# Kernel tuning notes

Hardware: AMD Instinct MI355X
Metric: run time of the kernel (lower is better)

Reference implementation:

```python
import jax, jax.numpy as jnp
import numpy as np

T, N, D = 8, 2048, 64
H, NH = 128, 4        # hidden_dim, num_heads (flax default num_heads=4)
HD = H // NH
TE = 16               # time_embedding_dim
OUT = 64              # final output_dim
E = D + TE            # enhanced node feature dim


def _params(key):
    ks = jax.random.split(key, 16)
    s = 0.05
    w = lambda k, shape: jax.random.normal(k, shape, jnp.float32) * s
    return dict(
        time_freq=w(ks[0], (T, TE // 2)) * 2.0,
        Wq=w(ks[1], (T, E, H)), bq=jnp.zeros((T, H), jnp.float32),
        Wk=w(ks[2], (T, E, H)), bk=jnp.zeros((T, H), jnp.float32),
        Wv=w(ks[3], (T, E, H)), bv=jnp.zeros((T, H), jnp.float32),
        ln_g=jnp.ones((T, H), jnp.float32), ln_b=jnp.zeros((T, H), jnp.float32),
        W1=w(ks[4], (T, H, 2 * H)), b1=jnp.zeros((T, 2 * H), jnp.float32),
        W2=w(ks[5], (T, 2 * H, H)), b2=jnp.zeros((T, H), jnp.float32),
        Wr=w(ks[6], (T, 2 * H, H)), br=jnp.zeros((T, H), jnp.float32),
        Wz=w(ks[7], (T, 2 * H, H)), bz=jnp.zeros((T, H), jnp.float32),
        Wn=w(ks[8], (T, 2 * H, H)), bn=jnp.zeros((T, H), jnp.float32),
        Wout=w(ks[9], (H, OUT)), bout=jnp.zeros((OUT,), jnp.float32),
    )


def setup_inputs() -> dict:
    key = jax.random.key(0)
    k0, k1, k2, k3, kp = jax.random.split(key, 5)
    inp = dict(
        node_sequence=jax.random.normal(k0, (T, N, D), jnp.float32),
        adjacency_sequence=(jax.random.uniform(k1, (T, N, N)) < 0.02).astype(jnp.float32),
        timestamps=jax.random.uniform(k2, (T, N), jnp.float32) * 100.0,
        edge_sequence=jax.random.randint(k3, (T, 32768, 2), 0, N),  # unused in math
    )
    inp.update(_params(kp))
    return inp


def _forward(node_sequence, adjacency_sequence, timestamps, time_freq,
             Wq, bq, Wk, bk, Wv, bv, ln_g, ln_b, W1, b1, W2, b2,
             Wr, br, Wz, bz, Wn, bn, Wout, bout):
    eye = jnp.eye(N, dtype=jnp.float32)
    inv_sqrt_hd = np.float32(1.0 / np.sqrt(HD))

    def step(h, xs):
        (nodes, adj, ts, tf, wq, bq_, wk, bk_, wv, bv_, g, b,
         w1, b1_, w2, b2_, wr, br_, wz, bz_, wn, bn_) = xs
        # sinusoidal time encoding -> enhanced node features [N, D+TE]
        ang = ts[:, None] * tf[None, :]
        enh = jnp.concatenate([nodes, jnp.sin(ang), jnp.cos(ang)], axis=-1)
        # the original builds per-head Dense projections in a Python loop;
        # concatenating them equals one [E,H] projection split into heads
        q = (enh @ wq + bq_).reshape(N, NH, HD)
        k = (enh @ wk + bk_).reshape(N, NH, HD)
        v = (enh @ wv + bv_).reshape(N, NH, HD)
        scores = jnp.einsum('nhd,mhd->hnm', q, k) * inv_sqrt_hd  # [NH,N,N]
        decay = jnp.exp(-jnp.abs(ts[:, None] - ts[None, :]) / 10.0)
        scores = scores * decay[None]
        mask = (adj + eye) > 0
        scores = jnp.where(mask[None], scores, -jnp.inf)
        attn = jax.nn.softmax(scores, axis=-1)
        mh = jnp.einsum('hnm,mhd->nhd', attn, v).reshape(N, H)
        # residual skipped: mh dim (128) != enhanced dim (80), as in source
        mu = mh.mean(-1, keepdims=True)
        var = mh.var(-1, keepdims=True)
        mh = (mh - mu) * jax.lax.rsqrt(var + 1e-6) * g + b  # LayerNorm eps=1e-6
        ff = jax.nn.gelu(mh @ w1 + b1_) @ w2 + b2_  # inner output_dim == hidden_dim
        # GRU cell
        hx = jnp.concatenate([h, ff], axis=-1)
        r = jax.nn.sigmoid(hx @ wr + br_)
        z = jax.nn.sigmoid(hx @ wz + bz_)
        n_ = jnp.tanh(jnp.concatenate([r * h, ff], axis=-1) @ wn + bn_)
        return (1.0 - z) * n_ + z * h, None

    xs = (node_sequence, adjacency_sequence, timestamps, time_freq,
          Wq, bq, Wk, bk, Wv, bv, ln_g, ln_b, W1, b1, W2, b2,
          Wr, br, Wz, bz, Wn, bn)
    h0 = jnp.zeros((N, H), jnp.float32)
    h, _ = jax.lax.scan(step, h0, xs)
    return h @ Wout + bout  # [N, OUT]


def reference(node_sequence, adjacency_sequence, timestamps, edge_sequence,
              time_freq, Wq, bq, Wk, bk, Wv, bv, ln_g, ln_b,
              W1, b1, W2, b2, Wr, br, Wz, bz, Wn, bn, Wout, bout):
    # edge_sequence is accepted by the original forward but never used
    return _forward(node_sequence, adjacency_sequence, timestamps, time_freq,
                    Wq, bq, Wk, bk, Wv, bv, ln_g, ln_b, W1, b1, W2, b2,
                    Wr, br, Wz, bz, Wn, bn, Wout, bout)
```

## Files before the change

### kernel.cpp

```cpp
#include <hip/hip_runtime.h>
#include <math.h>

#define T 8
#define N 2048
#define D 64
#define H 128
#define NH 4
#define HD 32
#define TE 16
#define OUT 64
#define E 80
#define NBCAP 128

typedef float f4v __attribute__((ext_vector_type(4)));
typedef __attribute__((ext_vector_type(8))) short bf16x8;
typedef __attribute__((ext_vector_type(4))) float f32x4;

__device__ __forceinline__ float gelu_tanh(float x){
    float x3 = x*x*x;
    float t = tanhf(0.7978845608028654f*(x + 0.044715f*x3));
    return 0.5f*x*(1.0f+t);
}
__device__ __forceinline__ float sigmoidf_(float x){ return 1.0f/(1.0f+expf(-x)); }
__device__ __forceinline__ unsigned short f2bf(float x){
    unsigned u = __float_as_uint(x);
    return (unsigned short)((u + 0x7FFFu + ((u>>16)&1u)) >> 16);
}
__device__ __forceinline__ float bf2f(unsigned short x){
    return __uint_as_float(((unsigned)x) << 16);
}

__global__ __launch_bounds__(256) void k_compact(
    const float* __restrict__ adj, unsigned short* __restrict__ nb, int* __restrict__ cnt)
{
    int wid  = threadIdx.x >> 6;
    int lane = threadIdx.x & 63;
    int row  = blockIdx.x*4 + wid;
    int n = row & 2047;
    const f4v* arow4 = (const f4v*)(adj + (size_t)row*(size_t)N);

    f4v a4[8];
    #pragma unroll
    for (int it=0; it<8; it++) a4[it] = __builtin_nontemporal_load(arow4 + it*64 + lane);

    unsigned short* nbr = nb + (size_t)row*NBCAP;
    int c = 0;
    unsigned long long lt = (1ull<<lane)-1ull;
    #pragma unroll
    for (int it = 0; it < 8; it++){
        int m0 = it*256 + lane*4;
        bool f0 = (a4[it].x>0.f) || (m0   == n);
        bool f1 = (a4[it].y>0.f) || (m0+1 == n);
        bool f2 = (a4[it].z>0.f) || (m0+2 == n);
        bool f3 = (a4[it].w>0.f) || (m0+3 == n);
        unsigned long long b0=__ballot(f0), b1=__ballot(f1), b2=__ballot(f2), b3=__ballot(f3);
        int before = __popcll(b0&lt)+__popcll(b1&lt)+__popcll(b2&lt)+__popcll(b3&lt);
        int pos = c + before;
        if (f0 && pos<NBCAP) nbr[pos] = (unsigned short)(m0  );  pos += f0;
        if (f1 && pos<NBCAP) nbr[pos] = (unsigned short)(m0+1);  pos += f1;
        if (f2 && pos<NBCAP) nbr[pos] = (unsigned short)(m0+2);  pos += f2;
        if (f3 && pos<NBCAP) nbr[pos] = (unsigned short)(m0+3);  pos += f3;
        c += __popcll(b0)+__popcll(b1)+__popcll(b2)+__popcll(b3);
    }
    if (lane == 0) cnt[row] = (c > NBCAP) ? NBCAP : c;
}

__global__ __launch_bounds__(64) void k_wswz(
    const float* __restrict__ W1, const float* __restrict__ W2,
    const float* __restrict__ Wr, const float* __restrict__ Wz, const float* __restrict__ Wn,
    unsigned short* __restrict__ W1s, unsigned short* __restrict__ W2s,
    unsigned short* __restrict__ Wrs, unsigned short* __restrict__ Wzs, unsigned short* __restrict__ Wns,
    unsigned short* __restrict__ Wrt, unsigned short* __restrict__ Wzt, unsigned short* __restrict__ Wnt)
{
    int b = blockIdx.x;
    const float* src; unsigned short* dst; int NT,KB,ncol,koff;
    if (b < 512)      {          src=W1; dst=W1s; NT=16; KB=4; ncol=256; koff=0;   }
    else if (b < 1024){ b-=512;  src=W2; dst=W2s; NT=8;  KB=8; ncol=128; koff=0;   }
    else if (b < 1280){ b-=1024; src=Wr; dst=Wrs; NT=8;  KB=4; ncol=128; koff=128; }
    else if (b < 1536){ b-=1280; src=Wz; dst=Wzs; NT=8;  KB=4; ncol=128; koff=128; }
    else if (b < 1792){ b-=1536; src=Wn; dst=Wns; NT=8;  KB=4; ncol=128; koff=128; }
    else if (b < 2048){ b-=1792; src=Wr; dst=Wrt; NT=8;  KB=4; ncol=128; koff=0;   }
    else if (b < 2304){ b-=2048; src=Wz; dst=Wzt; NT=8;  KB=4; ncol=128; koff=0;   }
    else              { b-=2304; src=Wn; dst=Wnt; NT=8;  KB=4; ncol=128; koff=0;   }
    int fpt = NT*KB;
    int t = b / fpt, rem = b % fpt, nt = rem / KB, kb = rem % KB;
    int lane = threadIdx.x;
    int kk = koff + kb*32 + (lane>>4)*8;
    int n  = nt*16 + (lane&15);
    const float* s = src + (size_t)t*32768;
    bf16x8 o;
    #pragma unroll
    for (int j=0;j<8;j++) o[j] = (short)f2bf(s[(size_t)(kk+j)*ncol + n]);
    *(bf16x8*)(dst + ((size_t)b*64 + lane)*8) = o;
}

__global__ __launch_bounds__(256) void k_qkv(
    const float* __restrict__ nodes, const float* __restrict__ ts, const float* __restrict__ tf,
    const float* __restrict__ Wq, const float* __restrict__ bq,
    const float* __restrict__ Wk, const float* __restrict__ bk,
    const float* __restrict__ Wv, const float* __restrict__ bv,
    float* __restrict__ q, float* __restrict__ k, float* __restrict__ v)
{
    const int BR = 16;
    __shared__ float A[BR*E];
    int t  = blockIdx.x >> 7;
    int n0 = (blockIdx.x & 127) * BR;
    int tid = threadIdx.x;
    for (int idx = tid; idx < BR*E; idx += 256){
        int r = idx / E, e = idx - r*E;
        int n = n0 + r;
        float val;
        if (e < D) val = nodes[((size_t)(t*N+n))*D + e];
        else {
            int j = (e - D) & 7;
            float ang = ts[t*N+n] * tf[t*(TE/2)+j];
            val = (e < D+8) ? sinf(ang) : cosf(ang);
        }
        A[idx] = val;
    }
    __syncthreads();
    for (int jj = tid; jj < 3*H; jj += 256){
        int sel = jj >> 7, j = jj & 127;
        const float* W = (sel==0?Wq:(sel==1?Wk:Wv)) + (size_t)t*E*H;
        const float* B = (sel==0?bq:(sel==1?bk:bv)) + t*H;
        float acc[BR];
        float bias = B[j];
        #pragma unroll
        for (int r=0;r<BR;r++) acc[r]=bias;
        for (int e=0;e<E;e+=4){
            float w0=W[(e+0)*H+j], w1=W[(e+1)*H+j], w2=W[(e+2)*H+j], w3=W[(e+3)*H+j];
            #pragma unroll
            for (int r=0;r<BR;r++){
                float4 a = *(const float4*)&A[r*E+e];
                acc[r] += a.x*w0 + a.y*w1 + a.z*w2 + a.w*w3;
            }
        }
        float* outp = (sel==0?q:(sel==1?k:v));
        #pragma unroll
        for (int r=0;r<BR;r++) outp[((size_t)(t*N+n0+r))*H + j] = acc[r];
    }
}

__global__ __launch_bounds__(256) void k_attn(
    const unsigned short* __restrict__ nb, const int* __restrict__ cntp,
    const float* __restrict__ ts,
    const float* __restrict__ q, const float* __restrict__ k, const float* __restrict__ v,
    const float* __restrict__ ln_g, const float* __restrict__ ln_b,
    float* __restrict__ mhn)
{
    __shared__ unsigned short nb_s[4][NBCAP];
    __shared__ float sc_s[4][64][NH];
    __shared__ float qrow_s[4][H];

    int wid  = threadIdx.x >> 6;
    int lane = threadIdx.x & 63;
    int t = blockIdx.x & 7;
    int n = (blockIdx.x >> 3)*4 + wid;
    int row = t*N + n;
    size_t rowbase = (size_t)row;
    float tsn = ts[row];
    int cnt = cntp[row];

    for (int i = lane; i < cnt; i += 64) nb_s[wid][i] = nb[rowbase*NBCAP + i];
    qrow_s[wid][lane]    = q[rowbase*H + lane];
    qrow_s[wid][lane+64] = q[rowbase*H + lane + 64];
    __builtin_amdgcn_wave_barrier();

    const float inv_sqrt_hd = 0.17677669529663687f;
    const float NEG = -3.402823466e38f;
    int g   = lane >> 4;
    int l16 = lane & 15;
    int hd  = l16 >> 2;
    int hh16 = lane >> 4;

    f4v q0 = *(const f4v*)&qrow_s[wid][l16*8];
    f4v q1 = *(const f4v*)&qrow_s[wid][l16*8+4];

    float mR0=NEG,mR1=NEG,mR2=NEG,mR3=NEG;
    float sR0=0.f,sR1=0.f,sR2=0.f,sR3=0.f;
    f4v accA = {0.f,0.f,0.f,0.f}, accB = {0.f,0.f,0.f,0.f};

    for (int cb = 0; cb < cnt; cb += 64){
        int cc = min(64, cnt - cb);
        for (int i0 = 0; i0 < cc; i0 += 4){
            int jn = i0 + g;
            bool act = jn < cc;
            float part = 0.f;
            int m = 0;
            if (act){
                m = nb_s[wid][cb + jn];
                const f4v* kp = (const f4v*)(k + ((size_t)t*N + m)*H + l16*8);
                f4v k0 = kp[0], k1 = kp[1];
                part = q0.x*k0.x + q0.y*k0.y + q0.z*k0.z + q0.w*k0.w
                     + q1.x*k1.x + q1.y*k1.y + q1.z*k1.z + q1.w*k1.w;
            }
            part += __shfl_xor(part, 1);
            part += __shfl_xor(part, 2);
            if (act && (l16 & 3) == 0){
                float dt = fabsf(tsn - ts[t*N + m]);
                float w  = expf(-dt*0.1f) * inv_sqrt_hd;
                sc_s[wid][jn][l16>>2] = part * w;
            }
        }
        __builtin_amdgcn_wave_barrier();
        float mx = NEG;
        for (int i = l16; i < cc; i += 16) mx = fmaxf(mx, sc_s[wid][i][hh16]);
        #pragma unroll
        for (int off=8; off; off>>=1) mx = fmaxf(mx, __shfl_xor(mx, off, 16));
        float h0m=__shfl(mx,0), h1m=__shfl(mx,16), h2m=__shfl(mx,32), h3m=__shfl(mx,48);
        float n0=fmaxf(mR0,h0m), n1=fmaxf(mR1,h1m), n2=fmaxf(mR2,h2m), n3=fmaxf(mR3,h3m);
        float e0=expf(mR0-n0), e1=expf(mR1-n1), e2=expf(mR2-n2), e3=expf(mR3-n3);
        float nh = (hh16==0)?n0:((hh16==1)?n1:((hh16==2)?n2:n3));
        float sum = 0.f;
        for (int i = l16; i < cc; i += 16){
            float p = expf(sc_s[wid][i][hh16] - nh);
            sc_s[wid][i][hh16] = p;
            sum += p;
        }
        #pragma unroll
        for (int off=8; off; off>>=1) sum += __shfl_xor(sum, off, 16);
        float su0=__shfl(sum,0), su1=__shfl(sum,16), su2=__shfl(sum,32), su3=__shfl(sum,48);
        sR0 = sR0*e0 + su0; sR1 = sR1*e1 + su1;
        sR2 = sR2*e2 + su2; sR3 = sR3*e3 + su3;
        mR0=n0; mR1=n1; mR2=n2; mR3=n3;
        float eh = (hd==0)?e0:((hd==1)?e1:((hd==2)?e2:e3));
        accA *= eh; accB *= eh;
        __builtin_amdgcn_wave_barrier();
        for (int i0 = 0; i0 < cc; i0 += 4){
            int jn = i0 + g;
            if (jn < cc){
                int m = nb_s[wid][cb + jn];
                const f4v* vp = (const f4v*)(v + ((size_t)t*N + m)*H + l16*8);
                f4v v0 = vp[0], v1 = vp[1];
                float p = sc_s[wid][jn][hd];
                accA += p * v0;
                accB += p * v1;
            }
        }
        __builtin_amdgcn_wave_barrier();
    }

    #pragma unroll
    for (int off = 16; off <= 32; off <<= 1){
        accA.x += __shfl_xor(accA.x, off); accA.y += __shfl_xor(accA.y, off);
        accA.z += __shfl_xor(accA.z, off); accA.w += __shfl_xor(accA.w, off);
        accB.x += __shfl_xor(accB.x, off); accB.y += __shfl_xor(accB.y, off);
        accB.z += __shfl_xor(accB.z, off); accB.w += __shfl_xor(accB.w, off);
    }
    float sh = (hd==0)?sR0:((hd==1)?sR1:((hd==2)?sR2:sR3));
    float inv = 1.f / sh;
    accA *= inv; accB *= inv;

    float ls = accA.x+accA.y+accA.z+accA.w + accB.x+accB.y+accB.z+accB.w;
    #pragma unroll
    for (int off=8; off; off>>=1) ls += __shfl_xor(ls, off, 16);
    float mu = ls * (1.f/128.f);
    f4v dA = accA - mu, dB = accB - mu;
    float vs = dA.x*dA.x+dA.y*dA.y+dA.z*dA.z+dA.w*dA.w
             + dB.x*dB.x+dB.y*dB.y+dB.z*dB.z+dB.w*dB.w;
    #pragma unroll
    for (int off=8; off; off>>=1) vs += __shfl_xor(vs, off, 16);
    float rs = rsqrtf(vs*(1.f/128.f) + 1e-6f);

    if (g == 0){
        const f4v* gp = (const f4v*)(ln_g + t*H + l16*8);
        const f4v* bp = (const f4v*)(ln_b + t*H + l16*8);
        f4v g0 = gp[0], g1 = gp[1], b0 = bp[0], b1 = bp[1];
        f4v o0 = dA*rs*g0 + b0;
        f4v o1 = dB*rs*g1 + b1;
        f4v* op = (f4v*)(mhn + rowbase*H + l16*8);
        op[0] = o0; op[1] = o1;
    }
}

#define ULD 264
__global__ __launch_bounds__(256) void k_ffpre(
    const float* __restrict__ mhn,
    const unsigned short* __restrict__ W1s, const float* __restrict__ b1,
    const unsigned short* __restrict__ W2s, const float* __restrict__ b2,
    const unsigned short* __restrict__ Wrs, const float* __restrict__ br,
    const unsigned short* __restrict__ Wzs, const float* __restrict__ bz,
    const unsigned short* __restrict__ Wns, const float* __restrict__ bn,
    unsigned short* __restrict__ fr, unsigned short* __restrict__ fz, unsigned short* __restrict__ fn)
{
    __shared__ unsigned short U_lds[32*ULD];
    int tid = threadIdx.x;
    int w = tid >> 6, lane = tid & 63;
    int t = blockIdx.x & 7;
    int n0 = (blockIdx.x >> 3) * 32;
    int li = lane & 15, ls = lane >> 4;

    bf16x8 af[2][4];
    const float* Abase = mhn + (size_t)(t*N + n0)*H;
    #pragma unroll
    for (int mt=0; mt<2; mt++){
        #pragma unroll
        for (int kb=0; kb<4; kb++){
            const float* p = Abase + (size_t)(mt*16 + li)*H + kb*32 + ls*8;
            float4 x0 = *(const float4*)p;
            float4 x1 = *(const float4*)(p+4);
            bf16x8 a;
            a[0]=(short)f2bf(x0.x); a[1]=(short)f2bf(x0.y); a[2]=(short)f2bf(x0.z); a[3]=(short)f2bf(x0.w);
            a[4]=(short)f2bf(x1.x); a[5]=(short)f2bf(x1.y); a[6]=(short)f2bf(x1.z); a[7]=(short)f2bf(x1.w);
            af[mt][kb] = a;
        }
    }

    const bf16x8* W1f = (const bf16x8*)W1s;
    #pragma unroll
    for (int u=0; u<4; u++){
        int nt = w*4 + u;
        f32x4 c0 = {0.f,0.f,0.f,0.f}, c1 = {0.f,0.f,0.f,0.f};
        #pragma unroll
        for (int kb=0; kb<4; kb++){
            bf16x8 b = W1f[((t*16 + nt)*4 + kb)*64 + lane];
            c0 = __builtin_amdgcn_mfma_f32_16x16x32_bf16(af[0][kb], b, c0, 0,0,0);
            c1 = __builtin_amdgcn_mfma_f32_16x16x32_bf16(af[1][kb], b, c1, 0,0,0);
        }
        float bias = b1[t*256 + nt*16 + li];
        #pragma unroll
        for (int i=0;i<4;i++){
            U_lds[(     ls*4+i)*ULD + nt*16 + li] = f2bf(gelu_tanh(c0[i] + bias));
            U_lds[(16 + ls*4+i)*ULD + nt*16 + li] = f2bf(gelu_tanh(c1[i] + bias));
        }
    }
    __syncthreads();

    const bf16x8* W2f = (const bf16x8*)W2s;
    f32x4 c2[2][2];
    #pragma unroll
    for (int u=0;u<2;u++){ c2[u][0] = (f32x4){0.f,0.f,0.f,0.f}; c2[u][1] = (f32x4){0.f,0.f,0.f,0.f}; }
    for (int kb=0; kb<8; kb++){
        bf16x8 a0 = *(const bf16x8*)&U_lds[(     li)*ULD + kb*32 + ls*8];
        bf16x8 a1 = *(const bf16x8*)&U_lds[(16 + li)*ULD + kb*32 + ls*8];
        #pragma unroll
        for (int u=0; u<2; u++){
            int nt = w*2 + u;
            bf16x8 b = W2f[((t*8 + nt)*8 + kb)*64 + lane];
            c2[u][0] = __builtin_amdgcn_mfma_f32_16x16x32_bf16(a0, b, c2[u][0], 0,0,0);
            c2[u][1] = __builtin_amdgcn_mfma_f32_16x16x32_bf16(a1, b, c2[u][1], 0,0,0);
        }
    }
    __syncthreads();
    #pragma unroll
    for (int u=0; u<2; u++){
        int nt = w*2 + u;
        float bias = b2[t*128 + nt*16 + li];
        #pragma unroll
        for (int i=0;i<4;i++){
            U_lds[(     ls*4+i)*ULD + nt*16 + li] = f2bf(c2[u][0][i] + bias);
            U_lds[(16 + ls*4+i)*ULD + nt*16 + li] = f2bf(c2[u][1][i] + bias);
        }
    }
    __syncthreads();

    bf16x8 aF[2][4];
    #pragma unroll
    for (int mt=0; mt<2; mt++)
        #pragma unroll
        for (int kb=0; kb<4; kb++)
            aF[mt][kb] = *(const bf16x8*)&U_lds[(mt*16 + li)*ULD + kb*32 + ls*8];

    #pragma unroll
    for (int u=0; u<6; u++){
        int unit = w*6 + u;
        int gate = unit >> 3, nt = unit & 7;
        const bf16x8* Wf = (const bf16x8*)(gate==0 ? Wrs : (gate==1 ? Wzs : Wns));
        const float*  Bv = gate==0 ? br : (gate==1 ? bz : bn);
        unsigned short* outp = gate==0 ? fr : (gate==1 ? fz : fn);
        f32x4 c0 = {0.f,0.f,0.f,0.f}, c1 = {0.f,0.f,0.f,0.f};
        #pragma unroll
        for (int kb=0; kb<4; kb++){
            bf16x8 b = Wf[((t*8 + nt)*4 + kb)*64 + lane];
            c0 = __builtin_amdgcn_mfma_f32_16x16x32_bf16(aF[0][kb], b, c0, 0,0,0);
            c1 = __builtin_amdgcn_mfma_f32_16x16x32_bf16(aF[1][kb], b, c1, 0,0,0);
        }
        float bias = Bv[t*128 + nt*16 + li];
        #pragma unroll
        for (int i=0;i<4;i++){
            outp[(size_t)(t*N + n0 +      ls*4+i)*H + nt*16 + li] = f2bf(c0[i] + bias);
            outp[(size_t)(t*N + n0 + 16 + ls*4+i)*H + nt*16 + li] = f2bf(c1[i] + bias);
        }
    }
}

#define HLD 132
__global__ __launch_bounds__(256) void k_gru_mfma(
    const unsigned short* __restrict__ fr, const unsigned short* __restrict__ fz,
    const unsigned short* __restrict__ fn,
    const unsigned short* __restrict__ Wrt, const unsigned short* __restrict__ Wzt,
    const unsigned short* __restrict__ Wnt,
    const float* __restrict__ Wout, const float* __restrict__ bout,
    float* __restrict__ out)
{
    __shared__ unsigned short fLDS[3*8*16*H];
    __shared__ float Hs[16*HLD], Zl[16*HLD], RH[16*HLD];
    int tid = threadIdx.x;
    int w = tid >> 6, lane = tid & 63;
    int li = lane & 15, ls = lane >> 4;
    int n0 = blockIdx.x * 16;
    int gateA = w >> 1;

    {
        const unsigned short* g0 = fr; const unsigned short* g1 = fz; const unsigned short* g2 = fn;
        #pragma unroll
        for (int t=0; t<T; t++){
            *(bf16x8*)&fLDS[(0*8+t)*2048 + tid*8] = *(const bf16x8*)(g0 + ((size_t)t*N+n0)*H + tid*8);
            *(bf16x8*)&fLDS[(1*8+t)*2048 + tid*8] = *(const bf16x8*)(g1 + ((size_t)t*N+n0)*H + tid*8);
            *(bf16x8*)&fLDS[(2*8+t)*2048 + tid*8] = *(const bf16x8*)(g2 + ((size_t)t*N+n0)*H + tid*8);
        }
    }
    for (int idx = tid; idx < 16*HLD; idx += 256) Hs[idx] = 0.f;
    __syncthreads();

    for (int t = 0; t < T; t++){
        bf16x8 af[4];
        #pragma unroll
        for (int kb=0; kb<4; kb++){
            const float* p = &Hs[li*HLD + kb*32 + ls*8];
            float4 x0 = *(const float4*)p, x1 = *(const float4*)(p+4);
            bf16x8 a;
            a[0]=(short)f2bf(x0.x); a[1]=(short)f2bf(x0.y); a[2]=(short)f2bf(x0.z); a[3]=(short)f2bf(x0.w);
            a[4]=(short)f2bf(x1.x); a[5]=(short)f2bf(x1.y); a[6]=(short)f2bf(x1.z); a[7]=(short)f2bf(x1.w);
            af[kb] = a;
        }
        const bf16x8* WfA = (const bf16x8*)(gateA ? Wzt : Wrt);
        const unsigned short* PA = &fLDS[(gateA*8 + t)*2048];
        #pragma unroll
        for (int u=0; u<4; u++){
            int nt = (w*4 + u) & 7;
            f32x4 c;
            #pragma unroll
            for (int i=0;i<4;i++) c[i] = bf2f(PA[(ls*4+i)*H + nt*16 + li]);
            #pragma unroll
            for (int kb=0; kb<4; kb++){
                bf16x8 b = WfA[((t*8 + nt)*4 + kb)*64 + lane];
                c = __builtin_amdgcn_mfma_f32_16x16x32_bf16(af[kb], b, c, 0,0,0);
            }
            #pragma unroll
            for (int i=0;i<4;i++){
                int idx = (ls*4+i)*HLD + nt*16 + li;
                float s = sigmoidf_(c[i]);
                if (gateA) Zl[idx] = s;
                else       RH[idx] = s * Hs[idx];
            }
        }
        __syncthreads();
        bf16x8 an[4];
        #pragma unroll
        for (int kb=0; kb<4; kb++){
            const float* p = &RH[li*HLD + kb*32 + ls*8];
            float4 x0 = *(const float4*)p, x1 = *(const float4*)(p+4);
            bf16x8 a;
            a[0]=(short)f2bf(x0.x); a[1]=(short)f2bf(x0.y); a[2]=(short)f2bf(x0.z); a[3]=(short)f2bf(x0.w);
            a[4]=(short)f2bf(x1.x); a[5]=(short)f2bf(x1.y); a[6]=(short)f2bf(x1.z); a[7]=(short)f2bf(x1.w);
            an[kb] = a;
        }
        const unsigned short* PC = &fLDS[(2*8 + t)*2048];
        #pragma unroll
        for (int u=0; u<2; u++){
            int nt = w*2 + u;
            f32x4 c;
            #pragma unroll
            for (int i=0;i<4;i++) c[i] = bf2f(PC[(ls*4+i)*H + nt*16 + li]);
            #pragma unroll
            for (int kb=0; kb<4; kb++){
                bf16x8 b = ((const bf16x8*)Wnt)[((t*8 + nt)*4 + kb)*64 + lane];
                c = __builtin_amdgcn_mfma_f32_16x16x32_bf16(an[kb], b, c, 0,0,0);
            }
            #pragma unroll
            for (int i=0;i<4;i++){
                int ridx = (ls*4+i)*HLD + nt*16 + li;
                float nv = tanhf(c[i]);
                float zz = Zl[ridx];
                Hs[ridx] = (1.f - zz)*nv + zz*Hs[ridx];
            }
        }
        __syncthreads();
    }

    {
        int j = tid & 63, rq = tid >> 6;
        #pragma unroll
        for (int rr=0; rr<4; rr++){
            int r = rq*4 + rr;
            float acc = bout[j];
            for (int e=0; e<H; e+=4){
                float4 a = *(const float4*)&Hs[r*HLD + e];
                acc += a.x*Wout[(e+0)*OUT+j] + a.y*Wout[(e+1)*OUT+j]
                     + a.z*Wout[(e+2)*OUT+j] + a.w*Wout[(e+3)*OUT+j];
            }
            out[(size_t)(n0 + r)*OUT + j] = acc;
        }
    }
}

extern "C" void kernel_launch(void* const* d_in, const int* in_sizes, int n_in,
                              void* d_out, int out_size, void* d_ws, size_t ws_size,
                              hipStream_t stream)
{
    const float* nodes = (const float*)d_in[0];
    const float* adj   = (const float*)d_in[1];
    const float* ts    = (const float*)d_in[2];
    const float* tf    = (const float*)d_in[4];
    const float* Wq = (const float*)d_in[5];  const float* bq = (const float*)d_in[6];
    const float* Wk = (const float*)d_in[7];  const float* bk = (const float*)d_in[8];
    const float* Wv = (const float*)d_in[9];  const float* bv = (const float*)d_in[10];
    const float* lng = (const float*)d_in[11]; const float* lnb = (const float*)d_in[12];
    const float* W1 = (const float*)d_in[13]; const float* b1 = (const float*)d_in[14];
    const float* W2 = (const float*)d_in[15]; const float* b2 = (const float*)d_in[16];
    const float* Wr = (const float*)d_in[17]; const float* br = (const float*)d_in[18];
    const float* Wz = (const float*)d_in[19]; const float* bz = (const float*)d_in[20];
    const float* Wn = (const float*)d_in[21]; const float* bn = (const float*)d_in[22];
    const float* Wout = (const float*)d_in[23]; const float* bout = (const float*)d_in[24];
    float* out = (float*)d_out;

    const size_t TNH = (size_t)T*N*H;
    float* ws  = (float*)d_ws;
    float* q   = ws;
    float* k   = q  + TNH;
    float* v   = k  + TNH;
    float* mhn = v  + TNH;
    unsigned short* frh = (unsigned short*)(mhn + TNH);
    unsigned short* fzh = frh + TNH;
    unsigned short* fnh = fzh + TNH;
    unsigned short* nb  = fnh + TNH;
    int* cnt = (int*)(nb + (size_t)T*N*NBCAP);
    unsigned short* W1s = (unsigned short*)(cnt + T*N);
    unsigned short* W2s = W1s + 262144;
    unsigned short* Wrs = W2s + 262144;
    unsigned short* Wzs = Wrs + 131072;
    unsigned short* Wns = Wzs + 131072;
    unsigned short* Wrt = Wns + 131072;
    unsigned short* Wzt = Wrt + 131072;
    unsigned short* Wnt = Wzt + 131072;

    k_wswz<<<dim3(2560), dim3(64), 0, stream>>>(W1,W2,Wr,Wz,Wn, W1s,W2s,Wrs,Wzs,Wns, Wrt,Wzt,Wnt);
    k_compact<<<dim3(T*N/4), dim3(256), 0, stream>>>(adj, nb, cnt);
    k_qkv<<<dim3(T*(N/16)), dim3(256), 0, stream>>>(nodes, ts, tf, Wq,bq, Wk,bk, Wv,bv, q,k,v);
    k_attn<<<dim3(T*N/4), dim3(256), 0, stream>>>(nb, cnt, ts, q,k,v, lng,lnb, mhn);
    k_ffpre<<<dim3(512), dim3(256), 0, stream>>>(mhn, W1s,b1, W2s,b2, Wrs,br, Wzs,bz, Wns,bn, frh,fzh,fnh);
    k_gru_mfma<<<dim3(N/16), dim3(256), 0, stream>>>(frh,fzh,fnh, Wrt,Wzt,Wnt, Wout,bout, out);
}
```

Before: 178.6 us.

## Fuse feed-forward and GRU input projections into the GRU kernel

Merges the feed-forward plus GRU input-projection kernel into the recurrent GRU kernel. Each 16-node block now computes the FF and gate pre-activations for all 8 timesteps and writes them straight into shared memory, removing the global bf16 fr/fz/fn intermediates and one kernel launch. In exchange, that work now runs on only 128 blocks (versus 512 before) with 16-row tiles. Weights are re-read per block, which reduces parallelism and MFMA reuse.

```diff
diff --git a/kernel.cpp b/kernel.cpp
--- a/kernel.cpp
+++ b/kernel.cpp
@@ -274,142 +274,101 @@
 }
 
 #define ULD 264
-__global__ __launch_bounds__(256) void k_ffpre(
+#define HLD 132
+__global__ __launch_bounds__(256) void k_ffgru(
     const float* __restrict__ mhn,
     const unsigned short* __restrict__ W1s, const float* __restrict__ b1,
     const unsigned short* __restrict__ W2s, const float* __restrict__ b2,
     const unsigned short* __restrict__ Wrs, const float* __restrict__ br,
     const unsigned short* __restrict__ Wzs, const float* __restrict__ bz,
     const unsigned short* __restrict__ Wns, const float* __restrict__ bn,
-    unsigned short* __restrict__ fr, unsigned short* __restrict__ fz, unsigned short* __restrict__ fn)
-{
-    __shared__ unsigned short U_lds[32*ULD];
-    int tid = threadIdx.x;
-    int w = tid >> 6, lane = tid & 63;
-    int t = blockIdx.x & 7;
-    int n0 = (blockIdx.x >> 3) * 32;
-    int li = lane & 15, ls = lane >> 4;
-
-    bf16x8 af[2][4];
-    const float* Abase = mhn + (size_t)(t*N + n0)*H;
-    #pragma unroll
-    for (int mt=0; mt<2; mt++){
-        #pragma unroll
-        for (int kb=0; kb<4; kb++){
-            const float* p = Abase + (size_t)(mt*16 + li)*H + kb*32 + ls*8;
-            float4 x0 = *(const float4*)p;
-            float4 x1 = *(const float4*)(p+4);
-            bf16x8 a;
-            a[0]=(short)f2bf(x0.x); a[1]=(short)f2bf(x0.y); a[2]=(short)f2bf(x0.z); a[3]=(short)f2bf(x0.w);
-            a[4]=(short)f2bf(x1.x); a[5]=(short)f2bf(x1.y); a[6]=(short)f2bf(x1.z); a[7]=(short)f2bf(x1.w);
-            af[mt][kb] = a;
-        }
-    }
-
-    const bf16x8* W1f = (const bf16x8*)W1s;
-    #pragma unroll
-    for (int u=0; u<4; u++){
-        int nt = w*4 + u;
-        f32x4 c0 = {0.f,0.f,0.f,0.f}, c1 = {0.f,0.f,0.f,0.f};
-        #pragma unroll
-        for (int kb=0; kb<4; kb++){
-            bf16x8 b = W1f[((t*16 + nt)*4 + kb)*64 + lane];
-            c0 = __builtin_amdgcn_mfma_f32_16x16x32_bf16(af[0][kb], b, c0, 0,0,0);
-            c1 = __builtin_amdgcn_mfma_f32_16x16x32_bf16(af[1][kb], b, c1, 0,0,0);
-        }
-        float bias = b1[t*256 + nt*16 + li];
-        #pragma unroll
-        for (int i=0;i<4;i++){
-            U_lds[(     ls*4+i)*ULD + nt*16 + li] = f2bf(gelu_tanh(c0[i] + bias));
-            U_lds[(16 + ls*4+i)*ULD + nt*16 + li] = f2bf(gelu_tanh(c1[i] + bias));
-        }
-    }
-    __syncthreads();
-
-    const bf16x8* W2f = (const bf16x8*)W2s;
-    f32x4 c2[2][2];
-    #pragma unroll
-    for (int u=0;u<2;u++){ c2[u][0] = (f32x4){0.f,0.f,0.f,0.f}; c2[u][1] = (f32x4){0.f,0.f,0.f,0.f}; }
-    for (int kb=0; kb<8; kb++){
-        bf16x8 a0 = *(const bf16x8*)&U_lds[(     li)*ULD + kb*32 + ls*8];
-        bf16x8 a1 = *(const bf16x8*)&U_lds[(16 + li)*ULD + kb*32 + ls*8];
-        #pragma unroll
-        for (int u=0; u<2; u++){
-            int nt = w*2 + u;
-            bf16x8 b = W2f[((t*8 + nt)*8 + kb)*64 + lane];
-            c2[u][0] = __builtin_amdgcn_mfma_f32_16x16x32_bf16(a0, b, c2[u][0], 0,0,0);
-            c2[u][1] = __builtin_amdgcn_mfma_f32_16x16x32_bf16(a1, b, c2[u][1], 0,0,0);
-        }
-    }
-    __syncthreads();
-    #pragma unroll
-    for (int u=0; u<2; u++){
-        int nt = w*2 + u;
-        float bias = b2[t*128 + nt*16 + li];
-        #pragma unroll
-        for (int i=0;i<4;i++){
-            U_lds[(     ls*4+i)*ULD + nt*16 + li] = f2bf(c2[u][0][i] + bias);
-            U_lds[(16 + ls*4+i)*ULD + nt*16 + li] = f2bf(c2[u][1][i] + bias);
-        }
-    }
-    __syncthreads();
-
-    bf16x8 aF[2][4];
-    #pragma unroll
-    for (int mt=0; mt<2; mt++)
-        #pragma unroll
-        for (int kb=0; kb<4; kb++)
-            aF[mt][kb] = *(const bf16x8*)&U_lds[(mt*16 + li)*ULD + kb*32 + ls*8];
-
-    #pragma unroll
-    for (int u=0; u<6; u++){
-        int unit = w*6 + u;
-        int gate = unit >> 3, nt = unit & 7;
-        const bf16x8* Wf = (const bf16x8*)(gate==0 ? Wrs : (gate==1 ? Wzs : Wns));
-        const float*  Bv = gate==0 ? br : (gate==1 ? bz : bn);
-        unsigned short* outp = gate==0 ? fr : (gate==1 ? fz : fn);
-        f32x4 c0 = {0.f,0.f,0.f,0.f}, c1 = {0.f,0.f,0.f,0.f};
-        #pragma unroll
-        for (int kb=0; kb<4; kb++){
-            bf16x8 b = Wf[((t*8 + nt)*4 + kb)*64 + lane];
-            c0 = __builtin_amdgcn_mfma_f32_16x16x32_bf16(aF[0][kb], b, c0, 0,0,0);
-            c1 = __builtin_amdgcn_mfma_f32_16x16x32_bf16(aF[1][kb], b, c1, 0,0,0);
-        }
-        float bias = Bv[t*128 + nt*16 + li];
-        #pragma unroll
-        for (int i=0;i<4;i++){
-            outp[(size_t)(t*N + n0 +      ls*4+i)*H + nt*16 + li] = f2bf(c0[i] + bias);
-            outp[(size_t)(t*N + n0 + 16 + ls*4+i)*H + nt*16 + li] = f2bf(c1[i] + bias);
-        }
-    }
-}
-
-#define HLD 132
-__global__ __launch_bounds__(256) void k_gru_mfma(
-    const unsigned short* __restrict__ fr, const unsigned short* __restrict__ fz,
-    const unsigned short* __restrict__ fn,
     const unsigned short* __restrict__ Wrt, const unsigned short* __restrict__ Wzt,
     const unsigned short* __restrict__ Wnt,
     const float* __restrict__ Wout, const float* __restrict__ bout,
     float* __restrict__ out)
 {
     __shared__ unsigned short fLDS[3*8*16*H];
+    __shared__ unsigned short U_lds[16*ULD];
     __shared__ float Hs[16*HLD], Zl[16*HLD], RH[16*HLD];
     int tid = threadIdx.x;
     int w = tid >> 6, lane = tid & 63;
     int li = lane & 15, ls = lane >> 4;
     int n0 = blockIdx.x * 16;
+
+    for (int t = 0; t < T; t++){
+        bf16x8 af[4];
+        #pragma unroll
+        for (int kb=0; kb<4; kb++){
+            const float* p = mhn + (size_t)(t*N + n0 + li)*H + kb*32 + ls*8;
+            float4 x0 = *(const float4*)p, x1 = *(const float4*)(p+4);
+            bf16x8 a;
+            a[0]=(short)f2bf(x0.x); a[1]=(short)f2bf(x0.y); a[2]=(short)f2bf(x0.z); a[3]=(short)f2bf(x0.w);
+            a[4]=(short)f2bf(x1.x); a[5]=(short)f2bf(x1.y); a[6]=(short)f2bf(x1.z); a[7]=(short)f2bf(x1.w);
+            af[kb] = a;
+        }
+        const bf16x8* W1f = (const bf16x8*)W1s;
+        #pragma unroll
+        for (int u=0; u<4; u++){
+            int nt = w*4 + u;
+            f32x4 c = {0.f,0.f,0.f,0.f};
+            #pragma unroll
+            for (int kb=0; kb<4; kb++){
+                bf16x8 b = W1f[((t*16 + nt)*4 + kb)*64 + lane];
+                c = __builtin_amdgcn_mfma_f32_16x16x32_bf16(af[kb], b, c, 0,0,0);
+            }
+            float bias = b1[t*256 + nt*16 + li];
+            #pragma unroll
+            for (int i=0;i<4;i++)
+                U_lds[(ls*4+i)*ULD + nt*16 + li] = f2bf(gelu_tanh(c[i] + bias));
+        }
+        __syncthreads();
+        const bf16x8* W2f = (const bf16x8*)W2s;
+        f32x4 c2[2];
+        c2[0] = (f32x4){0.f,0.f,0.f,0.f}; c2[1] = (f32x4){0.f,0.f,0.f,0.f};
+        for (int kb=0; kb<8; kb++){
+            bf16x8 a0 = *(const bf16x8*)&U_lds[li*ULD + kb*32 + ls*8];
+            #pragma unroll
+            for (int u=0; u<2; u++){
+                int nt = w*2 + u;
+                bf16x8 b = W2f[((t*8 + nt)*8 + kb)*64 + lane];
+                c2[u] = __builtin_amdgcn_mfma_f32_16x16x32_bf16(a0, b, c2[u], 0,0,0);
+            }
+        }
+        __syncthreads();
+        #pragma unroll
+        for (int u=0; u<2; u++){
+            int nt = w*2 + u;
+            float bias = b2[t*128 + nt*16 + li];
+            #pragma unroll
+            for (int i=0;i<4;i++)
+                U_lds[(ls*4+i)*ULD + nt*16 + li] = f2bf(c2[u][i] + bias);
+        }
+        __syncthreads();
+        bf16x8 aF[4];
+        #pragma unroll
+        for (int kb=0; kb<4; kb++)
+            aF[kb] = *(const bf16x8*)&U_lds[li*ULD + kb*32 + ls*8];
+        #pragma unroll
+        for (int u=0; u<6; u++){
+            int unit = w*6 + u;
+            int gate = unit >> 3, nt = unit & 7;
+            const bf16x8* Wf = (const bf16x8*)(gate==0 ? Wrs : (gate==1 ? Wzs : Wns));
+            const float*  Bv = gate==0 ? br : (gate==1 ? bz : bn);
+            f32x4 c = {0.f,0.f,0.f,0.f};
+            #pragma unroll
+            for (int kb=0; kb<4; kb++){
+                bf16x8 b = Wf[((t*8 + nt)*4 + kb)*64 + lane];
+                c = __builtin_amdgcn_mfma_f32_16x16x32_bf16(aF[kb], b, c, 0,0,0);
+            }
+            float bias = Bv[t*128 + nt*16 + li];
+            #pragma unroll
+            for (int i=0;i<4;i++)
+                fLDS[(gate*8+t)*2048 + (ls*4+i)*H + nt*16 + li] = f2bf(c[i] + bias);
+        }
+        __syncthreads();
+    }
+
     int gateA = w >> 1;
-
-    {
-        const unsigned short* g0 = fr; const unsigned short* g1 = fz; const unsigned short* g2 = fn;
-        #pragma unroll
-        for (int t=0; t<T; t++){
-            *(bf16x8*)&fLDS[(0*8+t)*2048 + tid*8] = *(const bf16x8*)(g0 + ((size_t)t*N+n0)*H + tid*8);
-            *(bf16x8*)&fLDS[(1*8+t)*2048 + tid*8] = *(const bf16x8*)(g1 + ((size_t)t*N+n0)*H + tid*8);
-            *(bf16x8*)&fLDS[(2*8+t)*2048 + tid*8] = *(const bf16x8*)(g2 + ((size_t)t*N+n0)*H + tid*8);
-        }
-    }
     for (int idx = tid; idx < 16*HLD; idx += 256) Hs[idx] = 0.f;
     __syncthreads();
 
@@ -521,10 +480,7 @@
     float* k   = q  + TNH;
     float* v   = k  + TNH;
     float* mhn = v  + TNH;
-    unsigned short* frh = (unsigned short*)(mhn + TNH);
-    unsigned short* fzh = frh + TNH;
-    unsigned short* fnh = fzh + TNH;
-    unsigned short* nb  = fnh + TNH;
+    unsigned short* nb = (unsigned short*)(mhn + TNH);
     int* cnt = (int*)(nb + (size_t)T*N*NBCAP);
     unsigned short* W1s = (unsigned short*)(cnt + T*N);
     unsigned short* W2s = W1s + 262144;
@@ -539,6 +495,6 @@
     k_compact<<<dim3(T*N/4), dim3(256), 0, stream>>>(adj, nb, cnt);
     k_qkv<<<dim3(T*(N/16)), dim3(256), 0, stream>>>(nodes, ts, tf, Wq,bq, Wk,bk, Wv,bv, q,k,v);
     k_attn<<<dim3(T*N/4), dim3(256), 0, stream>>>(nb, cnt, ts, q,k,v, lng,lnb, mhn);
-    k_ffpre<<<dim3(512), dim3(256), 0, stream>>>(mhn, W1s,b1, W2s,b2, Wrs,br, Wzs,bz, Wns,bn, frh,fzh,fnh);
-    k_gru_mfma<<<dim3(N/16), dim3(256), 0, stream>>>(frh,fzh,fnh, Wrt,Wzt,Wnt, Wout,bout, out);
-}
+    k_ffgru<<<dim3(N/16), dim3(256), 0, stream>>>(mhn, W1s,b1, W2s,b2, Wrs,br, Wzs,bz, Wns,bn,
+                                                  Wrt,Wzt,Wnt, Wout,bout, out);
+}
```

Result: slower. 211.4 us (+18.4%).
